# Kernel tuning notes

Measured on AMD Instinct MI355X. Metric: run time of the kernel, lower is better.

## Reference

```python
import jax, jax.numpy as jnp
import numpy as np

B, T, C = 4, 2048, 1024
N_HEAD = 16
HEAD_DIM = C // N_HEAD
SCALE = 1.0 / np.sqrt(HEAD_DIM).astype(np.float32)


def setup_inputs() -> dict:
    key = jax.random.key(0)
    ks = jax.random.split(key, 5)
    std = 1.0 / np.sqrt(C).astype(np.float32)
    return {
        "x": jax.random.normal(ks[0], (B, T, C), dtype=jnp.float32),
        "Wq": jax.random.normal(ks[1], (C, C), dtype=jnp.float32) * std,
        "Wk": jax.random.normal(ks[2], (C, C), dtype=jnp.float32) * std,
        "Wv": jax.random.normal(ks[3], (C, C), dtype=jnp.float32) * std,
        "Wo": jax.random.normal(ks[4], (C, C), dtype=jnp.float32) * std,
    }


def reference(x, Wq, Wk, Wv, Wo):
    # nn.Linear(x) == x @ W.T; projections then split heads: (B, H, T, D)
    def split_heads(t):
        return t.reshape(B, T, N_HEAD, HEAD_DIM).transpose(0, 2, 1, 3)

    q = split_heads(x @ Wq.T)
    k = split_heads(x @ Wk.T)
    v = split_heads(x @ Wv.T)

    att = jnp.einsum("bhqd,bhkd->bhqk", q, k) * SCALE  # (B, H, T, T)
    causal = jnp.tril(jnp.ones((T, T), dtype=bool))
    att = jnp.where(causal[None, None], att, -jnp.inf)
    att = jax.nn.softmax(att, axis=-1)
    # dropout = 0.0 (eval): identity
    y = jnp.einsum("bhqk,bhkd->bhqd", att, v)  # (B, H, T, D)
    y = y.transpose(0, 2, 1, 3).reshape(B, T, C)
    return y @ Wo.T
```

## Files before the change

kernel.cpp:

```cpp
#include <hip/hip_runtime.h>
#include <stdint.h>

#define B_SZ   4
#define T_SEQ  2048
#define C_DIM  1024
#define N_HEAD 16
#define HEAD_D 64
#define SCALE  0.125f
#define QSCALE 0.18033688011112042f

typedef unsigned short u16;
typedef unsigned int   u32;
typedef __bf16  bfv8  __attribute__((ext_vector_type(8)));
typedef float   f32x4 __attribute__((ext_vector_type(4)));

__device__ __forceinline__ float bf2f(u16 v) {
  union { u32 i; float f; } u; u.i = ((u32)v) << 16; return u.f;
}
__device__ __forceinline__ u16 f2bf(float f) {
  union { float f; u32 i; } u; u.f = f;
  u32 r = u.i + 0x7FFFu + ((u.i >> 16) & 1u);
  return (u16)(r >> 16);
}
__device__ __forceinline__ u32 pkbf16(float a, float b) {
  union { float f; u32 i; } ua, ub; ua.f = a; ub.f = b;
  return ((ua.i + 0x8000u) >> 16) | ((ub.i + 0x8000u) & 0xFFFF0000u);
}
__device__ __forceinline__ float fexp2(float x) {
#if __has_builtin(__builtin_amdgcn_exp2f)
  return __builtin_amdgcn_exp2f(x);
#else
  return __expf(x * 0.69314718f);
#endif
}
__device__ __forceinline__ void gload_lds16(const u16* g, u16* l) {
  __builtin_amdgcn_global_load_lds(
      (__attribute__((address_space(1))) void*)(void*)g,
      (__attribute__((address_space(3))) void*)(void*)l, 16, 0, 0);
}

__global__ __launch_bounds__(256) void cvt_kernel(const float* __restrict__ src,
                                                  u16* __restrict__ dst, int n4) {
  int i = blockIdx.x * 256 + threadIdx.x;
  if (i < n4) {
    float4 v = ((const float4*)src)[i];
    int2 o; o.x = (int)pkbf16(v.x, v.y); o.y = (int)pkbf16(v.z, v.w);
    ((int2*)dst)[i] = o;
  }
}
__global__ __launch_bounds__(256) void cvt_w_kernel(
    const float* __restrict__ W0, const float* __restrict__ W1,
    const float* __restrict__ W2, const float* __restrict__ W3,
    u16* __restrict__ dst) {
  const float* s = (blockIdx.y == 0) ? W0 : (blockIdx.y == 1) ? W1
                 : (blockIdx.y == 2) ? W2 : W3;
  u16* d = dst + (size_t)blockIdx.y * (C_DIM * C_DIM);
  int i = blockIdx.x * 256 + threadIdx.x;
  float4 v = ((const float4*)s)[i];
  int2 o; o.x = (int)pkbf16(v.x, v.y); o.y = (int)pkbf16(v.z, v.w);
  ((int2*)d)[i] = o;
}

__device__ __forceinline__ void gemm_core(const u16* __restrict__ A,
                                          const u16* __restrict__ Bw,
                                          int m0, int n0,
                                          f32x4 acc[4][4],
                                          u16* As, u16* Bs) {
  const int tid  = threadIdx.x;
  const int wave = tid >> 6;
  const int lane = tid & 63;
  const int lrow = lane >> 2;
  const int lcol = (lane & 3) * 8;
  const int frow = lane & 15;
  const int fk   = (lane >> 4) * 8;
  const int wm   = wave >> 1, wn = wave & 1;

  for (int k0 = 0; k0 < C_DIM; k0 += 32) {
    __syncthreads();
    const u16* ga = A + (size_t)(m0 + wave * 32 + lrow) * C_DIM + k0 + lcol;
    gload_lds16(ga,              As + (wave * 32) * 32);
    gload_lds16(ga + 16 * C_DIM, As + (wave * 32 + 16) * 32);
    const u16* gb = Bw + (size_t)(n0 + wave * 32 + lrow) * C_DIM + k0 + lcol;
    gload_lds16(gb,              Bs + (wave * 32) * 32);
    gload_lds16(gb + 16 * C_DIM, Bs + (wave * 32 + 16) * 32);
    __syncthreads();

    bfv8 af[4], bfr[4];
#pragma unroll
    for (int mt = 0; mt < 4; mt++)
      af[mt] = *(const bfv8*)(As + (wm * 64 + mt * 16 + frow) * 32 + fk);
#pragma unroll
    for (int nt = 0; nt < 4; nt++)
      bfr[nt] = *(const bfv8*)(Bs + (wn * 64 + nt * 16 + frow) * 32 + fk);
#pragma unroll
    for (int mt = 0; mt < 4; mt++)
#pragma unroll
      for (int nt = 0; nt < 4; nt++)
        acc[mt][nt] = __builtin_amdgcn_mfma_f32_16x16x32_bf16(
            af[mt], bfr[nt], acc[mt][nt], 0, 0, 0);
  }
}

__global__ __launch_bounds__(256) void gemm_qkv_kernel(
    const u16* __restrict__ X, const u16* __restrict__ Wq,
    const u16* __restrict__ Wk, const u16* __restrict__ Wv,
    u16* __restrict__ Qo, u16* __restrict__ Ko, u16* __restrict__ Vo) {
  __shared__ __align__(16) u16 smem[8192];
  u16* As = smem;
  u16* Bs = smem + 4096;
  const u16* W = (blockIdx.z == 0) ? Wq : (blockIdx.z == 1) ? Wk : Wv;
  u16* dst     = (blockIdx.z == 0) ? Qo : (blockIdx.z == 1) ? Ko : Vo;
  const int m0 = blockIdx.x * 128, n0 = blockIdx.y * 128;

  f32x4 acc[4][4];
#pragma unroll
  for (int i = 0; i < 4; i++)
#pragma unroll
    for (int j = 0; j < 4; j++) acc[i][j] = {0.f, 0.f, 0.f, 0.f};

  gemm_core(X, W, m0, n0, acc, As, Bs);

  const int lane = threadIdx.x & 63, wave = threadIdx.x >> 6;
  const int wm = wave >> 1, wn = wave & 1;
  const int quad = lane >> 4, col = lane & 15;

  if (blockIdx.z == 2) {
    __syncthreads();
    u16* buf = smem + wave * 2048;
#pragma unroll
    for (int c = 0; c < 2; c++) {
#pragma unroll
      for (int mt = 0; mt < 4; mt++)
#pragma unroll
        for (int nn = 0; nn < 2; nn++) {
          int nt = 2 * c + nn;
          int ln = nn * 16 + col;
          int g  = mt * 4 + quad;
          int gp = g ^ (ln & 15);
          int2 o;
          o.x = (int)pkbf16(acc[mt][nt][0], acc[mt][nt][1]);
          o.y = (int)pkbf16(acc[mt][nt][2], acc[mt][nt][3]);
          *(int2*)(buf + ln * 64 + gp * 4) = o;
        }
#pragma unroll
      for (int rr = 0; rr < 4; rr++) {
        int ln  = rr * 8 + (lane >> 3);
        int seg = lane & 7;
        int g0 = (2 * seg) ^ (ln & 15), g1 = (2 * seg + 1) ^ (ln & 15);
        int2 a  = *(const int2*)(buf + ln * 64 + g0 * 4);
        int2 bv = *(const int2*)(buf + ln * 64 + g1 * 4);
        int m = m0 + wm * 64 + seg * 8;
        int bb = m >> 11, t = m & (T_SEQ - 1);
        int n = n0 + wn * 64 + c * 32 + ln;
        int h = n >> 6, d = n & 63;
        int4 o; o.x = a.x; o.y = a.y; o.z = bv.x; o.w = bv.y;
        *(int4*)(Vo + (((size_t)(bb * N_HEAD + h) * HEAD_D + d) * T_SEQ + t)) = o;
      }
    }
  } else {
    const float sc = (blockIdx.z == 0) ? QSCALE : 1.0f;
#pragma unroll
    for (int mt = 0; mt < 4; mt++)
#pragma unroll
      for (int nt = 0; nt < 4; nt++)
#pragma unroll
        for (int r = 0; r < 4; r++) {
          int m = m0 + wm * 64 + mt * 16 + quad * 4 + r;
          int n = n0 + wn * 64 + nt * 16 + col;
          int b = m >> 11, t = m & (T_SEQ - 1);
          int h = n >> 6, d = n & 63;
          dst[((size_t)(b * N_HEAD + h) * T_SEQ + t) * HEAD_D + d] =
              f2bf(acc[mt][nt][r] * sc);
        }
  }
}

__global__ __launch_bounds__(256) void gemm_out_kernel(
    const u16* __restrict__ Y, const u16* __restrict__ Wo,
    float* __restrict__ Out) {
  __shared__ __align__(16) u16 smem[8192];
  u16* As = smem; u16* Bs = smem + 4096;
  const int m0 = blockIdx.x * 128, n0 = blockIdx.y * 128;

  f32x4 acc[4][4];
#pragma unroll
  for (int i = 0; i < 4; i++)
#pragma unroll
    for (int j = 0; j < 4; j++) acc[i][j] = {0.f, 0.f, 0.f, 0.f};

  gemm_core(Y, Wo, m0, n0, acc, As, Bs);

  const int lane = threadIdx.x & 63, wave = threadIdx.x >> 6;
  const int wm = wave >> 1, wn = wave & 1;
  const int quad = lane >> 4, col = lane & 15;
#pragma unroll
  for (int mt = 0; mt < 4; mt++)
#pragma unroll
    for (int nt = 0; nt < 4; nt++)
#pragma unroll
      for (int r = 0; r < 4; r++) {
        int m = m0 + wm * 64 + mt * 16 + quad * 4 + r;
        int n = n0 + wn * 64 + nt * 16 + col;
        Out[(size_t)m * C_DIM + n] = acc[mt][nt][r];
      }
}

#define ATT_Q 128

__global__ __launch_bounds__(256) void attn_kernel(
    const u16* __restrict__ Qg, const u16* __restrict__ Kg,
    const u16* __restrict__ Vtg, u16* __restrict__ Yg) {
  __shared__ __align__(16) u16 Qs[128 * 64];
  __shared__ __align__(16) u16 Ks[64 * 64];
  __shared__ __align__(16) u16 Vt[64 * 64];
  __shared__ __align__(16) u16 Ps[128 * 64];

  const int tid = threadIdx.x;
  const int wave = tid >> 6, lane = tid & 63;
  const int quad = lane >> 4, l15 = lane & 15;
  const int bh = blockIdx.x;
  const int b = bh >> 4, h = bh & 15;
  const int qt = gridDim.y - 1 - blockIdx.y;
  const int q0 = qt * ATT_Q;

  {
    const int row = tid >> 1;
    const int c0 = (tid & 1) * 32;
    const u16* gp = Qg + ((size_t)bh * T_SEQ + q0 + row) * HEAD_D + c0;
#pragma unroll
    for (int g = 0; g < 4; g++) {
      int4 v = *(const int4*)(gp + g * 8);
      int pg = ((c0 >> 3) + g) ^ (row & 7);
      *(int4*)(Qs + row * 64 + pg * 8) = v;
    }
  }
  __syncthreads();

  bfv8 qb[2][2];
#pragma unroll
  for (int nt = 0; nt < 2; nt++)
#pragma unroll
    for (int ks = 0; ks < 2; ks++) {
      int q = wave * 32 + nt * 16 + l15;
      int pg = (ks * 4 + quad) ^ (q & 7);
      qb[nt][ks] = *(const bfv8*)(Qs + q * 64 + pg * 8);
    }

  float m_i[2] = {-1e30f, -1e30f}, l_i[2] = {0.f, 0.f};
  f32x4 ao[4][2];
#pragma unroll
  for (int mt = 0; mt < 4; mt++)
#pragma unroll
    for (int nt = 0; nt < 2; nt++) ao[mt][nt] = {0.f, 0.f, 0.f, 0.f};

  const int ktmax = 2 * qt + 1;
  for (int kt = 0; kt <= ktmax; kt++) {
    __syncthreads();
    {
      const int row = tid >> 2;
      const int c0 = (tid & 3) * 16;
      const u16* gk = Kg  + ((size_t)bh * T_SEQ + kt * 64 + row) * HEAD_D + c0;
      const u16* gv = Vtg + ((size_t)bh * HEAD_D + row) * T_SEQ + kt * 64 + c0;
#pragma unroll
      for (int gg = 0; gg < 2; gg++) {
        int4 kv = *(const int4*)(gk + gg * 8);
        int4 vv = *(const int4*)(gv + gg * 8);
        int pg = ((c0 >> 3) + gg) ^ (row & 7);
        *(int4*)(Ks + row * 64 + pg * 8) = kv;
        *(int4*)(Vt + row * 64 + pg * 8) = vv;
      }
    }
    __syncthreads();

    f32x4 as[4][2];
#pragma unroll
    for (int mt = 0; mt < 4; mt++)
#pragma unroll
      for (int nt = 0; nt < 2; nt++) as[mt][nt] = {0.f, 0.f, 0.f, 0.f};
#pragma unroll
    for (int mt = 0; mt < 4; mt++) {
      bfv8 ka[2];
#pragma unroll
      for (int ks = 0; ks < 2; ks++) {
        int key = mt * 16 + l15;
        int pg = (ks * 4 + quad) ^ (key & 7);
        ka[ks] = *(const bfv8*)(Ks + key * 64 + pg * 8);
      }
#pragma unroll
      for (int nt = 0; nt < 2; nt++)
#pragma unroll
        for (int ks = 0; ks < 2; ks++)
          as[mt][nt] = __builtin_amdgcn_mfma_f32_16x16x32_bf16(
              ka[ks], qb[nt][ks], as[mt][nt], 0, 0, 0);
    }

    const bool diag = (kt >= 2 * qt);
#pragma unroll
    for (int nt = 0; nt < 2; nt++) {
      const int q_l = wave * 32 + nt * 16 + l15;
      const int q_g = q0 + q_l;
      float sv[16];
#pragma unroll
      for (int mt = 0; mt < 4; mt++)
#pragma unroll
        for (int r = 0; r < 4; r++) {
          float s = as[mt][nt][r];
          if (diag) {
            int key_g = kt * 64 + mt * 16 + quad * 4 + r;
            if (key_g > q_g) s = -1e30f;
          }
          sv[mt * 4 + r] = s;
        }
      float rm = sv[0];
#pragma unroll
      for (int i = 1; i < 16; i++) rm = fmaxf(rm, sv[i]);
      rm = fmaxf(rm, __shfl_xor(rm, 16));
      rm = fmaxf(rm, __shfl_xor(rm, 32));
      float mn = fmaxf(m_i[nt], rm);
      float alpha = fexp2(m_i[nt] - mn);
      m_i[nt] = mn;
      float rs = 0.f;
      float pv[16];
#pragma unroll
      for (int i = 0; i < 16; i++) {
        float p = fexp2(sv[i] - mn);
        pv[i] = p;
        rs += p;
      }
      rs += __shfl_xor(rs, 16);
      rs += __shfl_xor(rs, 32);
      l_i[nt] = l_i[nt] * alpha + rs;
#pragma unroll
      for (int mt = 0; mt < 4; mt++) ao[mt][nt] *= alpha;
#pragma unroll
      for (int mt = 0; mt < 4; mt++) {
        int pg = (2 * mt + (quad >> 1)) ^ (q_l & 7);
        int2 o;
        o.x = (int)pkbf16(pv[mt * 4 + 0], pv[mt * 4 + 1]);
        o.y = (int)pkbf16(pv[mt * 4 + 2], pv[mt * 4 + 3]);
        *(int2*)(Ps + q_l * 64 + pg * 8 + (quad & 1) * 4) = o;
      }
    }
    __syncthreads();

    bfv8 pf[2][2];
#pragma unroll
    for (int nt = 0; nt < 2; nt++)
#pragma unroll
      for (int ks = 0; ks < 2; ks++) {
        int q_l = wave * 32 + nt * 16 + l15;
        int pg = (ks * 4 + quad) ^ (q_l & 7);
        pf[nt][ks] = *(const bfv8*)(Ps + q_l * 64 + pg * 8);
      }
#pragma unroll
    for (int mt = 0; mt < 4; mt++) {
      bfv8 va[2];
#pragma unroll
      for (int ks = 0; ks < 2; ks++) {
        int d = mt * 16 + l15;
        int pg = (ks * 4 + quad) ^ (d & 7);
        va[ks] = *(const bfv8*)(Vt + d * 64 + pg * 8);
      }
#pragma unroll
      for (int nt = 0; nt < 2; nt++)
#pragma unroll
        for (int ks = 0; ks < 2; ks++)
          ao[mt][nt] = __builtin_amdgcn_mfma_f32_16x16x32_bf16(
              va[ks], pf[nt][ks], ao[mt][nt], 0, 0, 0);
    }
  }

  __syncthreads();
#pragma unroll
  for (int nt = 0; nt < 2; nt++) {
    float inv = 1.0f / l_i[nt];
    int q_l = wave * 32 + nt * 16 + l15;
#pragma unroll
    for (int mt = 0; mt < 4; mt++) {
      int g = mt * 4 + quad;
      int gp = g ^ (q_l & 15);
      int2 o;
      o.x = (int)pkbf16(ao[mt][nt][0] * inv, ao[mt][nt][1] * inv);
      o.y = (int)pkbf16(ao[mt][nt][2] * inv, ao[mt][nt][3] * inv);
      *(int2*)(Qs + q_l * 64 + gp * 4) = o;
    }
  }
  __syncthreads();
#pragma unroll
  for (int rr = 0; rr < 4; rr++) {
    int q   = rr * 32 + (tid >> 3);
    int seg = tid & 7;
    int g0 = (2 * seg) ^ (q & 15), g1 = (2 * seg + 1) ^ (q & 15);
    int2 a  = *(const int2*)(Qs + q * 64 + g0 * 4);
    int2 bv = *(const int2*)(Qs + q * 64 + g1 * 4);
    int4 o; o.x = a.x; o.y = a.y; o.z = bv.x; o.w = bv.y;
    *(int4*)(Yg + ((size_t)b * T_SEQ + q0 + q) * C_DIM + h * HEAD_D + seg * 8) = o;
  }
}

extern "C" void kernel_launch(void* const* d_in, const int* in_sizes, int n_in,
                              void* d_out, int out_size, void* d_ws, size_t ws_size,
                              hipStream_t stream) {
  const float* x  = (const float*)d_in[0];
  const float* Wq = (const float*)d_in[1];
  const float* Wk = (const float*)d_in[2];
  const float* Wv = (const float*)d_in[3];
  const float* Wo = (const float*)d_in[4];
  float* out = (float*)d_out;

  const size_t NE = (size_t)B_SZ * T_SEQ * C_DIM;
  const size_t NW = (size_t)C_DIM * C_DIM;
  u16* xbf = (u16*)d_ws;
  u16* wqb = xbf + NE;
  u16* wkb = wqb + NW;
  u16* wvb = wkb + NW;
  u16* wob = wvb + NW;
  u16* qws = wob + NW;
  u16* kws = qws + NE;
  u16* vws = kws + NE;
  u16* yws = vws + NE;

  cvt_kernel<<<(int)(NE / 4 / 256), 256, 0, stream>>>(x, xbf, (int)(NE / 4));
  cvt_w_kernel<<<dim3((int)(NW / 4 / 256), 4), 256, 0, stream>>>(Wq, Wk, Wv, Wo, wqb);

  dim3 g1(T_SEQ * B_SZ / 128, C_DIM / 128, 3);
  gemm_qkv_kernel<<<g1, 256, 0, stream>>>(xbf, wqb, wkb, wvb, qws, kws, vws);

  dim3 g2(B_SZ * N_HEAD, T_SEQ / ATT_Q);
  attn_kernel<<<g2, 256, 0, stream>>>(qws, kws, vws, yws);

  dim3 g3(T_SEQ * B_SZ / 128, C_DIM / 128);
  gemm_out_kernel<<<g3, 256, 0, stream>>>(yws, wob, out);
}
```

Measured before the change: 280.7 us.

## Stage GEMM epilogues through LDS, prefetch K/V in registers, reorder attention tiles

The QKV and output GEMM epilogues now stage results in shared memory so each wave writes coalesced 16-byte rows, replacing scattered 2-byte and 4-byte global stores. The attention kernel prefetches the next K/V tile into registers while computing the current one. It also reuses the Q buffer for P, which drops a 16 KB array and one barrier per iteration, since each wave reads only its own P rows. It adds a launch_bounds occupancy hint and interleaves causal query tiles across the grid to balance work. The costs are doubled shared memory in the GEMM kernels, extra register pressure from the prefetch, and a switch from round-to-nearest-even to round-half-up bf16 conversion.

```diff
diff --git a/kernel.cpp b/kernel.cpp
--- a/kernel.cpp
+++ b/kernel.cpp
@@ -6,7 +6,6 @@
 #define C_DIM  1024
 #define N_HEAD 16
 #define HEAD_D 64
-#define SCALE  0.125f
 #define QSCALE 0.18033688011112042f
 
 typedef unsigned short u16;
@@ -14,13 +13,9 @@
 typedef __bf16  bfv8  __attribute__((ext_vector_type(8)));
 typedef float   f32x4 __attribute__((ext_vector_type(4)));
 
-__device__ __forceinline__ float bf2f(u16 v) {
-  union { u32 i; float f; } u; u.i = ((u32)v) << 16; return u.f;
-}
-__device__ __forceinline__ u16 f2bf(float f) {
+__device__ __forceinline__ u16 f2bf_hu(float f) {
   union { float f; u32 i; } u; u.f = f;
-  u32 r = u.i + 0x7FFFu + ((u.i >> 16) & 1u);
-  return (u16)(r >> 16);
+  return (u16)((u.i + 0x8000u) >> 16);
 }
 __device__ __forceinline__ u32 pkbf16(float a, float b) {
   union { float f; u32 i; } ua, ub; ua.f = a; ub.f = b;
@@ -105,9 +100,8 @@
     const u16* __restrict__ X, const u16* __restrict__ Wq,
     const u16* __restrict__ Wk, const u16* __restrict__ Wv,
     u16* __restrict__ Qo, u16* __restrict__ Ko, u16* __restrict__ Vo) {
-  __shared__ __align__(16) u16 smem[8192];
-  u16* As = smem;
-  u16* Bs = smem + 4096;
+  __shared__ __align__(16) u16 smem[16384];
+  u16* As = smem; u16* Bs = smem + 4096;
   const u16* W = (blockIdx.z == 0) ? Wq : (blockIdx.z == 1) ? Wk : Wv;
   u16* dst     = (blockIdx.z == 0) ? Qo : (blockIdx.z == 1) ? Ko : Vo;
   const int m0 = blockIdx.x * 128, n0 = blockIdx.y * 128;
@@ -119,43 +113,39 @@
     for (int j = 0; j < 4; j++) acc[i][j] = {0.f, 0.f, 0.f, 0.f};
 
   gemm_core(X, W, m0, n0, acc, As, Bs);
+  __syncthreads();
 
   const int lane = threadIdx.x & 63, wave = threadIdx.x >> 6;
   const int wm = wave >> 1, wn = wave & 1;
   const int quad = lane >> 4, col = lane & 15;
+  u16* buf = smem + wave * 4096;
+  const int bb = (m0 + wm * 64) >> 11;
+  const int t0 = (m0 + wm * 64) & (T_SEQ - 1);
+  const int h  = (n0 >> 6) + wn;
 
   if (blockIdx.z == 2) {
-    __syncthreads();
-    u16* buf = smem + wave * 2048;
-#pragma unroll
-    for (int c = 0; c < 2; c++) {
-#pragma unroll
-      for (int mt = 0; mt < 4; mt++)
-#pragma unroll
-        for (int nn = 0; nn < 2; nn++) {
-          int nt = 2 * c + nn;
-          int ln = nn * 16 + col;
-          int g  = mt * 4 + quad;
-          int gp = g ^ (ln & 15);
-          int2 o;
-          o.x = (int)pkbf16(acc[mt][nt][0], acc[mt][nt][1]);
-          o.y = (int)pkbf16(acc[mt][nt][2], acc[mt][nt][3]);
-          *(int2*)(buf + ln * 64 + gp * 4) = o;
-        }
-#pragma unroll
-      for (int rr = 0; rr < 4; rr++) {
-        int ln  = rr * 8 + (lane >> 3);
-        int seg = lane & 7;
-        int g0 = (2 * seg) ^ (ln & 15), g1 = (2 * seg + 1) ^ (ln & 15);
-        int2 a  = *(const int2*)(buf + ln * 64 + g0 * 4);
-        int2 bv = *(const int2*)(buf + ln * 64 + g1 * 4);
-        int m = m0 + wm * 64 + seg * 8;
-        int bb = m >> 11, t = m & (T_SEQ - 1);
-        int n = n0 + wn * 64 + c * 32 + ln;
-        int h = n >> 6, d = n & 63;
-        int4 o; o.x = a.x; o.y = a.y; o.z = bv.x; o.w = bv.y;
-        *(int4*)(Vo + (((size_t)(bb * N_HEAD + h) * HEAD_D + d) * T_SEQ + t)) = o;
-      }
+#pragma unroll
+    for (int mt = 0; mt < 4; mt++)
+#pragma unroll
+      for (int nt = 0; nt < 4; nt++) {
+        int d_l = nt * 16 + col;
+        int g   = mt * 4 + quad;
+        int gp  = g ^ (d_l & 15);
+        int2 o;
+        o.x = (int)pkbf16(acc[mt][nt][0], acc[mt][nt][1]);
+        o.y = (int)pkbf16(acc[mt][nt][2], acc[mt][nt][3]);
+        *(int2*)(buf + d_l * 64 + gp * 4) = o;
+      }
+#pragma unroll
+    for (int tt = 0; tt < 8; tt++) {
+      int d_l = tt * 8 + (lane >> 3);
+      int seg = lane & 7;
+      int g0 = (2 * seg) ^ (d_l & 15), g1 = (2 * seg + 1) ^ (d_l & 15);
+      int2 a  = *(const int2*)(buf + d_l * 64 + g0 * 4);
+      int2 bv = *(const int2*)(buf + d_l * 64 + g1 * 4);
+      int4 o; o.x = a.x; o.y = a.y; o.z = bv.x; o.w = bv.y;
+      *(int4*)(Vo + (((size_t)(bb * N_HEAD + h) * HEAD_D + d_l) * T_SEQ
+                     + t0 + seg * 8)) = o;
     }
   } else {
     const float sc = (blockIdx.z == 0) ? QSCALE : 1.0f;
@@ -165,20 +155,27 @@
       for (int nt = 0; nt < 4; nt++)
 #pragma unroll
         for (int r = 0; r < 4; r++) {
-          int m = m0 + wm * 64 + mt * 16 + quad * 4 + r;
-          int n = n0 + wn * 64 + nt * 16 + col;
-          int b = m >> 11, t = m & (T_SEQ - 1);
-          int h = n >> 6, d = n & 63;
-          dst[((size_t)(b * N_HEAD + h) * T_SEQ + t) * HEAD_D + d] =
-              f2bf(acc[mt][nt][r] * sc);
+          int m_l = mt * 16 + quad * 4 + r;
+          int n_l = nt * 16 + col;
+          int gp = (n_l >> 3) ^ (m_l & 7);
+          buf[m_l * 64 + gp * 8 + (n_l & 7)] = f2bf_hu(acc[mt][nt][r] * sc);
         }
+#pragma unroll
+    for (int tt = 0; tt < 8; tt++) {
+      int m_l = tt * 8 + (lane >> 3);
+      int seg = lane & 7;
+      int gp = seg ^ (m_l & 7);
+      int4 o = *(const int4*)(buf + m_l * 64 + gp * 8);
+      *(int4*)(dst + (((size_t)(bb * N_HEAD + h) * T_SEQ + t0 + m_l) * HEAD_D
+                      + seg * 8)) = o;
+    }
   }
 }
 
 __global__ __launch_bounds__(256) void gemm_out_kernel(
     const u16* __restrict__ Y, const u16* __restrict__ Wo,
     float* __restrict__ Out) {
-  __shared__ __align__(16) u16 smem[8192];
+  __shared__ __align__(16) u16 smem[16384];
   u16* As = smem; u16* Bs = smem + 4096;
   const int m0 = blockIdx.x * 128, n0 = blockIdx.y * 128;
 
@@ -189,38 +186,56 @@
     for (int j = 0; j < 4; j++) acc[i][j] = {0.f, 0.f, 0.f, 0.f};
 
   gemm_core(Y, Wo, m0, n0, acc, As, Bs);
+  __syncthreads();
 
   const int lane = threadIdx.x & 63, wave = threadIdx.x >> 6;
   const int wm = wave >> 1, wn = wave & 1;
   const int quad = lane >> 4, col = lane & 15;
-#pragma unroll
-  for (int mt = 0; mt < 4; mt++)
-#pragma unroll
-    for (int nt = 0; nt < 4; nt++)
-#pragma unroll
-      for (int r = 0; r < 4; r++) {
-        int m = m0 + wm * 64 + mt * 16 + quad * 4 + r;
-        int n = n0 + wn * 64 + nt * 16 + col;
-        Out[(size_t)m * C_DIM + n] = acc[mt][nt][r];
-      }
+  float* bufF = (float*)(smem + wave * 4096);
+
+#pragma unroll
+  for (int c = 0; c < 2; c++) {
+#pragma unroll
+    for (int mt = 0; mt < 4; mt++)
+#pragma unroll
+      for (int nn = 0; nn < 2; nn++)
+#pragma unroll
+        for (int r = 0; r < 4; r++) {
+          int nt = 2 * c + nn;
+          int m_l = mt * 16 + quad * 4 + r;
+          int n_l = nn * 16 + col;
+          int gp = (n_l >> 2) ^ (m_l & 7);
+          bufF[m_l * 32 + gp * 4 + (n_l & 3)] = acc[mt][nt][r];
+        }
+#pragma unroll
+    for (int tt = 0; tt < 8; tt++) {
+      int m_l = tt * 8 + (lane >> 3);
+      int seg = lane & 7;
+      int gp = seg ^ (m_l & 7);
+      float4 o = *(const float4*)(bufF + m_l * 32 + gp * 4);
+      *(float4*)(Out + (size_t)(m0 + wm * 64 + m_l) * C_DIM
+                 + n0 + wn * 64 + c * 32 + seg * 4) = o;
+    }
+  }
 }
 
 #define ATT_Q 128
 
-__global__ __launch_bounds__(256) void attn_kernel(
+__global__ __launch_bounds__(256, 4) void attn_kernel(
     const u16* __restrict__ Qg, const u16* __restrict__ Kg,
     const u16* __restrict__ Vtg, u16* __restrict__ Yg) {
-  __shared__ __align__(16) u16 Qs[128 * 64];
+  __shared__ __align__(16) u16 QPs[128 * 64];
   __shared__ __align__(16) u16 Ks[64 * 64];
   __shared__ __align__(16) u16 Vt[64 * 64];
-  __shared__ __align__(16) u16 Ps[128 * 64];
 
   const int tid = threadIdx.x;
   const int wave = tid >> 6, lane = tid & 63;
   const int quad = lane >> 4, l15 = lane & 15;
   const int bh = blockIdx.x;
   const int b = bh >> 4, h = bh & 15;
-  const int qt = gridDim.y - 1 - blockIdx.y;
+  const int yy = blockIdx.y, gq = yy >> 2, rq = yy & 3;
+  const int qt = (gq == 0) ? 15 - rq : (gq == 1) ? rq
+               : (gq == 2) ? 11 - rq : 4 + rq;
   const int q0 = qt * ATT_Q;
 
   {
@@ -231,7 +246,7 @@
     for (int g = 0; g < 4; g++) {
       int4 v = *(const int4*)(gp + g * 8);
       int pg = ((c0 >> 3) + g) ^ (row & 7);
-      *(int4*)(Qs + row * 64 + pg * 8) = v;
+      *(int4*)(QPs + row * 64 + pg * 8) = v;
     }
   }
   __syncthreads();
@@ -243,7 +258,7 @@
     for (int ks = 0; ks < 2; ks++) {
       int q = wave * 32 + nt * 16 + l15;
       int pg = (ks * 4 + quad) ^ (q & 7);
-      qb[nt][ks] = *(const bfv8*)(Qs + q * 64 + pg * 8);
+      qb[nt][ks] = *(const bfv8*)(QPs + q * 64 + pg * 8);
     }
 
   float m_i[2] = {-1e30f, -1e30f}, l_i[2] = {0.f, 0.f};
@@ -252,25 +267,31 @@
   for (int mt = 0; mt < 4; mt++)
 #pragma unroll
     for (int nt = 0; nt < 2; nt++) ao[mt][nt] = {0.f, 0.f, 0.f, 0.f};
+
+  const int srow = tid >> 2;
+  const int sc0 = (tid & 3) * 16;
+  const u16* gkb = Kg  + (size_t)bh * T_SEQ * HEAD_D + (size_t)srow * HEAD_D + sc0;
+  const u16* gvb = Vtg + (size_t)bh * HEAD_D * T_SEQ + (size_t)srow * T_SEQ + sc0;
+  const int pg0 = (sc0 >> 3) ^ (srow & 7), pg1 = ((sc0 >> 3) + 1) ^ (srow & 7);
+
+  int4 kr0, kr1, vr0, vr1;
+  kr0 = *(const int4*)(gkb);      kr1 = *(const int4*)(gkb + 8);
+  vr0 = *(const int4*)(gvb);      vr1 = *(const int4*)(gvb + 8);
 
   const int ktmax = 2 * qt + 1;
   for (int kt = 0; kt <= ktmax; kt++) {
     __syncthreads();
-    {
-      const int row = tid >> 2;
-      const int c0 = (tid & 3) * 16;
-      const u16* gk = Kg  + ((size_t)bh * T_SEQ + kt * 64 + row) * HEAD_D + c0;
-      const u16* gv = Vtg + ((size_t)bh * HEAD_D + row) * T_SEQ + kt * 64 + c0;
-#pragma unroll
-      for (int gg = 0; gg < 2; gg++) {
-        int4 kv = *(const int4*)(gk + gg * 8);
-        int4 vv = *(const int4*)(gv + gg * 8);
-        int pg = ((c0 >> 3) + gg) ^ (row & 7);
-        *(int4*)(Ks + row * 64 + pg * 8) = kv;
-        *(int4*)(Vt + row * 64 + pg * 8) = vv;
-      }
-    }
+    *(int4*)(Ks + srow * 64 + pg0 * 8) = kr0;
+    *(int4*)(Ks + srow * 64 + pg1 * 8) = kr1;
+    *(int4*)(Vt + srow * 64 + pg0 * 8) = vr0;
+    *(int4*)(Vt + srow * 64 + pg1 * 8) = vr1;
     __syncthreads();
+    if (kt < ktmax) {
+      const u16* gk = gkb + (size_t)(kt + 1) * 64 * HEAD_D;
+      const u16* gv = gvb + (kt + 1) * 64;
+      kr0 = *(const int4*)(gk);  kr1 = *(const int4*)(gk + 8);
+      vr0 = *(const int4*)(gv);  vr1 = *(const int4*)(gv + 8);
+    }
 
     f32x4 as[4][2];
 #pragma unroll
@@ -338,10 +359,9 @@
         int2 o;
         o.x = (int)pkbf16(pv[mt * 4 + 0], pv[mt * 4 + 1]);
         o.y = (int)pkbf16(pv[mt * 4 + 2], pv[mt * 4 + 3]);
-        *(int2*)(Ps + q_l * 64 + pg * 8 + (quad & 1) * 4) = o;
-      }
-    }
-    __syncthreads();
+        *(int2*)(QPs + q_l * 64 + pg * 8 + (quad & 1) * 4) = o;
+      }
+    }
 
     bfv8 pf[2][2];
 #pragma unroll
@@ -350,7 +370,7 @@
       for (int ks = 0; ks < 2; ks++) {
         int q_l = wave * 32 + nt * 16 + l15;
         int pg = (ks * 4 + quad) ^ (q_l & 7);
-        pf[nt][ks] = *(const bfv8*)(Ps + q_l * 64 + pg * 8);
+        pf[nt][ks] = *(const bfv8*)(QPs + q_l * 64 + pg * 8);
       }
 #pragma unroll
     for (int mt = 0; mt < 4; mt++) {
@@ -382,7 +402,7 @@
       int2 o;
       o.x = (int)pkbf16(ao[mt][nt][0] * inv, ao[mt][nt][1] * inv);
       o.y = (int)pkbf16(ao[mt][nt][2] * inv, ao[mt][nt][3] * inv);
-      *(int2*)(Qs + q_l * 64 + gp * 4) = o;
+      *(int2*)(QPs + q_l * 64 + gp * 4) = o;
     }
   }
   __syncthreads();
@@ -391,8 +411,8 @@
     int q   = rr * 32 + (tid >> 3);
     int seg = tid & 7;
     int g0 = (2 * seg) ^ (q & 15), g1 = (2 * seg + 1) ^ (q & 15);
-    int2 a  = *(const int2*)(Qs + q * 64 + g0 * 4);
-    int2 bv = *(const int2*)(Qs + q * 64 + g1 * 4);
+    int2 a  = *(const int2*)(QPs + q * 64 + g0 * 4);
+    int2 bv = *(const int2*)(QPs + q * 64 + g1 * 4);
     int4 o; o.x = a.x; o.y = a.y; o.z = bv.x; o.w = bv.y;
     *(int4*)(Yg + ((size_t)b * T_SEQ + q0 + q) * C_DIM + h * HEAD_D + seg * 8) = o;
   }
```

New measurement: 273.7 us. -2.5%, faster.
